# Kernel tuning notes

Hardware: AMD Instinct MI355X
Metric: run time of the kernel (lower is better)

The kernel has to match this reference:

```python
import jax, jax.numpy as jnp
import numpy as np

N_NODES = 50000
N_EDGES = 600000
DIM = 128
VOCAB = 512
PAD_ID = 0
LN_EPS = 1e-5


def setup_inputs() -> dict:
    key = jax.random.key(0)
    ks = jax.random.split(key, 8)
    node_ids = jax.random.randint(ks[0], (N_NODES,), 0, VOCAB, dtype=jnp.int32)
    edge_index = jax.random.randint(ks[1], (2, N_EDGES), 0, N_NODES, dtype=jnp.int32)
    edge_weight = jax.random.uniform(ks[2], (N_EDGES,), dtype=jnp.float32)
    # embedding with padding row zeroed (padding_idx semantics)
    emb = jax.random.normal(ks[3], (VOCAB, DIM), dtype=jnp.float32) * 0.05
    emb = emb.at[PAD_ID].set(0.0)
    s = 1.0 / np.sqrt(DIM)
    W1 = jax.random.normal(ks[4], (DIM, DIM), dtype=jnp.float32) * s
    b1 = jnp.zeros((DIM,), jnp.float32)
    W2 = jax.random.normal(ks[5], (DIM, DIM), dtype=jnp.float32) * s
    b2 = jnp.zeros((DIM,), jnp.float32)
    return {
        "node_ids": node_ids, "edge_index": edge_index, "edge_weight": edge_weight,
        "emb": emb, "W1": W1, "b1": b1, "W2": W2, "b2": b2,
        "gamma1": jnp.ones((DIM,), jnp.float32), "beta1": jnp.zeros((DIM,), jnp.float32),
        "gamma2": jnp.ones((DIM,), jnp.float32), "beta2": jnp.zeros((DIM,), jnp.float32),
    }


def _gcn_conv(x, row, col, ew, W, b, n_nodes):
    """PyG GCNConv: normalize=True, add_self_loops=True, improved=False.
    Aggregation j->i: edge (row=src j, col=dst i)."""
    h = x @ W  # [N, out]
    # add self loops with weight 1
    loop = jnp.arange(n_nodes, dtype=row.dtype)
    row_f = jnp.concatenate([row, loop])
    col_f = jnp.concatenate([col, loop])
    ew_f = jnp.concatenate([ew, jnp.ones((n_nodes,), ew.dtype)])
    # symmetric degree normalization (deg over destination index)
    deg = jax.ops.segment_sum(ew_f, col_f, num_segments=n_nodes)
    dis = jnp.where(deg > 0, jax.lax.rsqrt(jnp.maximum(deg, 1e-12)), 0.0)
    norm = dis[row_f] * ew_f * dis[col_f]  # [E+N]
    msg = norm[:, None] * h[row_f]  # gather + scale  [E+N, out]
    out = jax.ops.segment_sum(msg, col_f, num_segments=n_nodes)  # scatter-add
    return out + b


def _layer_norm(x, gamma, beta):
    mu = jnp.mean(x, axis=-1, keepdims=True)
    var = jnp.mean(jnp.square(x - mu), axis=-1, keepdims=True)
    return (x - mu) * jax.lax.rsqrt(var + LN_EPS) * gamma + beta


def reference(node_ids, edge_index, edge_weight, emb, W1, b1, W2, b2,
              gamma1, beta1, gamma2, beta2):
    row, col = edge_index[0], edge_index[1]
    x = emb[node_ids]  # [N, D]
    x1 = _gcn_conv(x, row, col, edge_weight, W1, b1, N_NODES)
    x = _layer_norm(x + x1, gamma1, beta1)  # dropout is identity in eval
    x2 = _gcn_conv(x, row, col, edge_weight, W2, b2, N_NODES)
    x = _layer_norm(x + x2, gamma2, beta2)
    return x
```

## Files before the change

kernel.cpp:

```cpp
#include <hip/hip_runtime.h>

#define N_NODES 50000
#define N_EDGES 600000
#define DIM     128
#define VOCAB   512
#define LN_EPS  1e-5f
#define FIXS    16777216.0f
#define BCAP    64

typedef unsigned int uint;
typedef unsigned long long ull;
typedef unsigned short ushort;
typedef unsigned char uchar;
typedef __attribute__((ext_vector_type(8))) short s8v;
typedef __attribute__((ext_vector_type(4))) float f4v;
typedef __attribute__((ext_vector_type(4))) int   i4v;
typedef __attribute__((ext_vector_type(4))) uint  u4v;
typedef __attribute__((ext_vector_type(2))) int   i2v;
typedef __attribute__((ext_vector_type(4))) float fv4;
typedef __attribute__((ext_vector_type(2))) float f2v;

__device__ __forceinline__ uint f2bf(float f) {
    uint u = __float_as_uint(f);
    return (u + 0x7fffu + ((u >> 16) & 1u)) >> 16;
}
__device__ __forceinline__ float bf_lo(uint p) { return __uint_as_float(p << 16); }
__device__ __forceinline__ float bf_hi(uint p) { return __uint_as_float(p & 0xffff0000u); }
__device__ __forceinline__ float dis_of(ull pv) {
    return rsqrtf(1.0f + (float)(uint)(pv & 0xffffffffu) * (1.0f / FIXS));
}

__global__ __launch_bounds__(256) void deg_mm1_kernel(
        const int* __restrict__ ei, const float* __restrict__ ew,
        ull* pack, ushort* __restrict__ rank, int E,
        const float* __restrict__ X, const float* __restrict__ W,
        uint* __restrict__ Hb, int M,
        const float* __restrict__ W2, ushort* __restrict__ Wp) {
    __shared__ float Wt[32 * 128];
    __shared__ float Xt[64 * 36];
    int tid = threadIdx.x;
    int nbDeg = (E / 8 + 255) / 256;
    int nmm = (M + 63) / 64;
    if ((int)blockIdx.x < nbDeg) {
        int e0 = (blockIdx.x * 256 + tid) * 8;
        if (e0 >= E) return;
        i4v c0 = __builtin_nontemporal_load((const i4v*)(ei + E + e0));
        i4v c1 = __builtin_nontemporal_load((const i4v*)(ei + E + e0 + 4));
        fv4 w0 = __builtin_nontemporal_load((const fv4*)(ew + e0));
        fv4 w1 = __builtin_nontemporal_load((const fv4*)(ew + e0 + 4));
        int   c[8] = {c0.x, c0.y, c0.z, c0.w, c1.x, c1.y, c1.z, c1.w};
        float w[8] = {w0.x, w0.y, w0.z, w0.w, w1.x, w1.y, w1.z, w1.w};
        ull r[8];
        #pragma unroll
        for (int k = 0; k < 8; k++) {
            ull a = (1ull << 32) | (ull)(uint)__float2int_rn(w[k] * FIXS);
            r[k] = atomicAdd(&pack[c[k]], a);
        }
        u4v o;
        o.x = (uint)(r[0] >> 32) | ((uint)(r[1] >> 32) << 16);
        o.y = (uint)(r[2] >> 32) | ((uint)(r[3] >> 32) << 16);
        o.z = (uint)(r[4] >> 32) | ((uint)(r[5] >> 32) << 16);
        o.w = (uint)(r[6] >> 32) | ((uint)(r[7] >> 32) << 16);
        __builtin_nontemporal_store(o, (u4v*)(rank + e0));
        return;
    }
    if ((int)blockIdx.x >= nbDeg + nmm) {
        int o = (blockIdx.x - nbDeg - nmm) * 256 + tid;
        int j = o & 7, lane = (o >> 3) & 63, chunk = o >> 9;
        int kc = chunk & 3, nc = chunk >> 2;
        int k = kc * 32 + (lane >> 4) * 8 + j;
        int n = nc * 16 + (lane & 15);
        Wp[o] = (ushort)f2bf(W2[k * 128 + n]);
        return;
    }
    int bx = blockIdx.x - nbDeg;
    int tx = tid & 31, ty = tid >> 5;
    int r0 = bx * 64;
    float acc[8][4];
    #pragma unroll
    for (int j = 0; j < 8; j++)
        #pragma unroll
        for (int c = 0; c < 4; c++) acc[j][c] = 0.f;

    for (int kb = 0; kb < 128; kb += 32) {
        __syncthreads();
        #pragma unroll
        for (int q = 0; q < 4; q++) {
            int f = q * 256 + tid;
            ((float4*)Wt)[f] = *(const float4*)(W + kb * 128 + f * 4);
        }
        #pragma unroll
        for (int q = 0; q < 2; q++) {
            int f = q * 256 + tid;
            int row = f >> 3, cs = f & 7;
            int gr = r0 + row;
            float4 xv = make_float4(0.f, 0.f, 0.f, 0.f);
            if (gr < M) xv = *(const float4*)(X + (size_t)gr * 128 + kb + cs * 4);
            *(float4*)(Xt + row * 36 + cs * 4) = xv;
        }
        __syncthreads();
        #pragma unroll
        for (int k = 0; k < 32; k += 4) {
            float wv[4][4];
            #pragma unroll
            for (int kk = 0; kk < 4; kk++) {
                float4 t4 = *(const float4*)(Wt + (k + kk) * 128 + tx * 4);
                wv[kk][0] = t4.x; wv[kk][1] = t4.y; wv[kk][2] = t4.z; wv[kk][3] = t4.w;
            }
            #pragma unroll
            for (int j = 0; j < 8; j++) {
                float4 xv = *(const float4*)(Xt + (ty * 8 + j) * 36 + k);
                float xs[4] = {xv.x, xv.y, xv.z, xv.w};
                #pragma unroll
                for (int kk = 0; kk < 4; kk++)
                    #pragma unroll
                    for (int c = 0; c < 4; c++)
                        acc[j][c] = fmaf(xs[kk], wv[kk][c], acc[j][c]);
            }
        }
    }
    #pragma unroll
    for (int j = 0; j < 8; j++) {
        int gr = r0 + ty * 8 + j;
        if (gr < M) {
            uint p0 = f2bf(acc[j][0]) | (f2bf(acc[j][1]) << 16);
            uint p1 = f2bf(acc[j][2]) | (f2bf(acc[j][3]) << 16);
            ((uint2*)Hb)[(size_t)gr * 32 + tx] = make_uint2(p0, p1);
        }
    }
}

__global__ void scatter_kernel(const int* __restrict__ ei, const float* __restrict__ ew,
                               const ull* __restrict__ pack, const int* __restrict__ nid,
                               const ushort* __restrict__ rank,
                               int2* __restrict__ epack, int E) {
    int e0 = (blockIdx.x * blockDim.x + threadIdx.x) * 4;
    if (e0 >= E) return;
    int4    s4 = *(const int4*)   (ei + e0);
    int4    c4 = *(const int4*)   (ei + E + e0);
    float4  w4 = *(const float4*) (ew + e0);
    ushort4 r4 = *(const ushort4*)(rank + e0);
    int   s[4] = {s4.x, s4.y, s4.z, s4.w};
    int   c[4] = {c4.x, c4.y, c4.z, c4.w};
    float w[4] = {w4.x, w4.y, w4.z, w4.w};
    int   r[4] = {r4.x, r4.y, r4.z, r4.w};
    #pragma unroll
    for (int k = 0; k < 4; k++) {
        ull ps = pack[s[k]];
        float dls = dis_of(ps);
        int pos = c[k] * BCAP + r[k];
        uint ids = (uint)s[k] | ((uint)nid[s[k]] << 16);
        epack[pos] = make_int2((int)ids, __float_as_int(dls * w[k]));
    }
}

__global__ __launch_bounds__(256) void mm2_mfma(const uint* __restrict__ Xb,
                                                const ushort* __restrict__ Wp,
                                                char* __restrict__ H8,
                                                float* __restrict__ rowscale, int M) {
    int wid = (blockIdx.x * 256 + threadIdx.x) >> 6;
    int lane = threadIdx.x & 63;
    int r0 = wid * 16;
    if (r0 >= M) return;
    int quad = lane >> 4, lo = lane & 15;
    const uint* xrow = Xb + (size_t)(r0 + lo) * 64 + quad * 4;
    s8v a[4];
    #pragma unroll
    for (int kc = 0; kc < 4; kc++) a[kc] = *(const s8v*)(xrow + kc * 16);
    f4v acc[8];
    #pragma unroll
    for (int nc = 0; nc < 8; nc++) {
        acc[nc] = (f4v){0.f, 0.f, 0.f, 0.f};
        #pragma unroll
        for (int kc = 0; kc < 4; kc++) {
            s8v b = *(const s8v*)(Wp + (size_t)((nc * 4 + kc) * 64 + lane) * 8);
            acc[nc] = __builtin_amdgcn_mfma_f32_16x16x32_bf16(a[kc], b, acc[nc], 0, 0, 0);
        }
    }
    float m[4];
    #pragma unroll
    for (int r = 0; r < 4; r++) {
        m[r] = 0.f;
        #pragma unroll
        for (int nc = 0; nc < 8; nc++) m[r] = fmaxf(m[r], fabsf(acc[nc][r]));
    }
    #pragma unroll
    for (int o = 1; o <= 8; o <<= 1)
        #pragma unroll
        for (int r = 0; r < 4; r++) m[r] = fmaxf(m[r], __shfl_xor(m[r], o, 64));
    #pragma unroll
    for (int r = 0; r < 4; r++) {
        float inv = (m[r] > 0.f) ? 127.0f / m[r] : 0.f;
        if (lo == 0) rowscale[r0 + quad * 4 + r] = m[r] * (1.0f / 127.0f);
        char* hp = H8 + (size_t)(r0 + quad * 4 + r) * 128 + lo;
        #pragma unroll
        for (int nc = 0; nc < 8; nc++)
            hp[nc * 16] = (char)__float2int_rn(acc[nc][r] * inv);
    }
}

template<int SHIFT, bool RESID_BF, bool OUT_BF, bool GI8>
__global__ __launch_bounds__(256) void agg_ln(const ull* __restrict__ pack,
                                              const int2* __restrict__ epack,
                                              const void* __restrict__ hb,
                                              const float* __restrict__ rowscale,
                                              const int* __restrict__ nid,
                                              const void* __restrict__ resid,
                                              const float* __restrict__ bias,
                                              const float* __restrict__ gamma,
                                              const float* __restrict__ beta,
                                              void* __restrict__ out, int n) {
    int i = (blockIdx.x * 256 + threadIdx.x) >> 6;
    int lane = threadIdx.x & 63;
    if (i >= n) return;
    int iw = __builtin_amdgcn_readfirstlane(i);
    ull pv = pack[iw];
    int deg = (int)(pv >> 32);
    float dl = dis_of(pv);
    int hri = nid ? nid[iw] : iw;
    float slo, shi;
    if (GI8) {
        uint ps = ((const ushort*)hb)[(size_t)hri * 64 + lane];
        float sc = rowscale[hri];
        slo = sc * (float)(signed char)(ps & 0xffu);
        shi = sc * (float)(signed char)(ps >> 8);
    } else {
        uint ps = ((const uint*)hb)[(size_t)hri * 64 + lane];
        slo = bf_lo(ps); shi = bf_hi(ps);
    }
    float sx[4] = {dl * slo, 0.f, 0.f, 0.f};
    float sy[4] = {dl * shi, 0.f, 0.f, 0.f};
    const int2* ep = epack + (size_t)iw * BCAP;
    for (int j = 0; j < deg; j += 8) {
        int2 er[8];
        #pragma unroll
        for (int k = 0; k < 8; k++) {
            int idx = (j + k < deg) ? j + k : deg - 1;
            er[k] = ep[idx];
        }
        uint qv[8];
        float sc[8];
        #pragma unroll
        for (int k = 0; k < 8; k++) {
            size_t row = ((uint)er[k].x >> SHIFT) & 0xffffu;
            if (GI8) {
                qv[k] = ((const ushort*)hb)[row * 64 + lane];
                sc[k] = rowscale[row];
            } else {
                qv[k] = ((const uint*)hb)[row * 64 + lane];
            }
        }
        #pragma unroll
        for (int k = 0; k < 8; k++) {
            float w = (j + k < deg) ? __int_as_float(er[k].y) : 0.f;
            float lo, hi;
            if (GI8) {
                w *= sc[k];
                lo = (float)(signed char)(qv[k] & 0xffu);
                hi = (float)(signed char)(qv[k] >> 8);
            } else {
                lo = bf_lo(qv[k]); hi = bf_hi(qv[k]);
            }
            sx[k & 3] += w * lo;
            sy[k & 3] += w * hi;
        }
    }
    float acc0 = (sx[0] + sx[1]) + (sx[2] + sx[3]);
    float acc1 = (sy[0] + sy[1]) + (sy[2] + sy[3]);
    float2 xr;
    if (RESID_BF) {
        uint pr = __builtin_nontemporal_load((const uint*)resid + (size_t)hri * 64 + lane);
        xr = make_float2(bf_lo(pr), bf_hi(pr));
    } else {
        xr = ((const float2*)resid)[(size_t)hri * 64 + lane];
    }
    float2 bi = ((const float2*)bias)[lane];
    float v0 = xr.x + dl * acc0 + bi.x;
    float v1 = xr.y + dl * acc1 + bi.y;
    float s1 = v0 + v1, s2 = v0 * v0 + v1 * v1;
    #pragma unroll
    for (int o = 32; o > 0; o >>= 1) {
        s1 += __shfl_xor(s1, o, 64);
        s2 += __shfl_xor(s2, o, 64);
    }
    float mu   = s1 * (1.0f / DIM);
    float var  = s2 * (1.0f / DIM) - mu * mu;
    float rstd = rsqrtf(var + LN_EPS);
    float2 ga = ((const float2*)gamma)[lane];
    float2 be = ((const float2*)beta)[lane];
    float o0 = (v0 - mu) * rstd * ga.x + be.x;
    float o1 = (v1 - mu) * rstd * ga.y + be.y;
    if (OUT_BF) {
        __builtin_nontemporal_store(f2bf(o0) | (f2bf(o1) << 16),
                                    (uint*)out + (size_t)i * 64 + lane);
    } else {
        f2v ov = {o0, o1};
        __builtin_nontemporal_store(ov, (f2v*)((float2*)out + (size_t)i * 64 + lane));
    }
}

extern "C" void kernel_launch(void* const* d_in, const int* in_sizes, int n_in,
                              void* d_out, int out_size, void* d_ws, size_t ws_size,
                              hipStream_t stream) {
    const int*   node_ids = (const int*)  d_in[0];
    const int*   ei       = (const int*)  d_in[1];
    const float* ew       = (const float*)d_in[2];
    const float* emb      = (const float*)d_in[3];
    const float* W1       = (const float*)d_in[4];
    const float* b1       = (const float*)d_in[5];
    const float* W2       = (const float*)d_in[6];
    const float* b2       = (const float*)d_in[7];
    const float* g1       = (const float*)d_in[8];
    const float* be1      = (const float*)d_in[9];
    const float* g2       = (const float*)d_in[10];
    const float* be2      = (const float*)d_in[11];
    float* out = (float*)d_out;

    char* p = (char*)d_ws;
    auto alloc = [&](size_t bytes) {
        char* r = p;
        p += (bytes + 255) & ~(size_t)255;
        return r;
    };
    char*   h8      = (char*)  alloc((size_t)N_NODES * DIM);
    float*  rsc     = (float*) alloc((size_t)N_NODES * 4);
    uint*   x1b     = (uint*)  alloc((size_t)N_NODES * 64 * 4);
    uint*   hembB   = (uint*)  alloc((size_t)VOCAB * 64 * 4);
    ushort* Wp      = (ushort*)alloc((size_t)128 * 128 * 2);
    ull*    pack    = (ull*)   alloc((size_t)N_NODES * 8);
    ushort* rank    = (ushort*)alloc((size_t)N_EDGES * 2);
    int2*   epack   = (int2*)  alloc((size_t)N_NODES * BCAP * 8);

    int nbDeg = (N_EDGES / 8 + 255) / 256;
    int nmm = (VOCAB + 63) / 64;

    (void)hipMemsetAsync(pack, 0, (size_t)N_NODES * 8, stream);
    deg_mm1_kernel<<<nbDeg + nmm + 64, 256, 0, stream>>>(
        ei, ew, pack, rank, N_EDGES, emb, W1, hembB, VOCAB, W2, Wp);

    scatter_kernel<<<(N_EDGES / 4 + 255) / 256, 256, 0, stream>>>(
        ei, ew, pack, node_ids, rank, epack, N_EDGES);

    agg_ln<16, false, true, false><<<(N_NODES + 3) / 4, 256, 0, stream>>>(
        pack, epack, hembB, nullptr, node_ids, emb, b1, g1, be1, x1b, N_NODES);

    mm2_mfma<<<(N_NODES / 16 + 3) / 4, 256, 0, stream>>>(x1b, Wp, h8, rsc, N_NODES);
    agg_ln<0, true, false, true><<<(N_NODES + 3) / 4, 256, 0, stream>>>(
        pack, epack, h8, rsc, nullptr, x1b, b2, g2, be2, out, N_NODES);
}
```

Baseline: 213.0 us.

## Fuse edge bucketing into degree atomics and defer source normalization to aggregation

```diff
diff --git a/kernel.cpp b/kernel.cpp
--- a/kernel.cpp
+++ b/kernel.cpp
@@ -15,8 +15,6 @@
 typedef __attribute__((ext_vector_type(8))) short s8v;
 typedef __attribute__((ext_vector_type(4))) float f4v;
 typedef __attribute__((ext_vector_type(4))) int   i4v;
-typedef __attribute__((ext_vector_type(4))) uint  u4v;
-typedef __attribute__((ext_vector_type(2))) int   i2v;
 typedef __attribute__((ext_vector_type(4))) float fv4;
 typedef __attribute__((ext_vector_type(2))) float f2v;
 
@@ -32,36 +30,39 @@
 
 __global__ __launch_bounds__(256) void deg_mm1_kernel(
         const int* __restrict__ ei, const float* __restrict__ ew,
-        ull* pack, ushort* __restrict__ rank, int E,
+        ull* pack, const int* __restrict__ nid, int2* __restrict__ epack, int E,
         const float* __restrict__ X, const float* __restrict__ W,
         uint* __restrict__ Hb, int M,
         const float* __restrict__ W2, ushort* __restrict__ Wp) {
     __shared__ float Wt[32 * 128];
     __shared__ float Xt[64 * 36];
     int tid = threadIdx.x;
-    int nbDeg = (E / 8 + 255) / 256;
+    int nbDeg = (E / 4 + 255) / 256;
     int nmm = (M + 63) / 64;
     if ((int)blockIdx.x < nbDeg) {
-        int e0 = (blockIdx.x * 256 + tid) * 8;
+        int e0 = (blockIdx.x * 256 + tid) * 4;
         if (e0 >= E) return;
-        i4v c0 = __builtin_nontemporal_load((const i4v*)(ei + E + e0));
-        i4v c1 = __builtin_nontemporal_load((const i4v*)(ei + E + e0 + 4));
-        fv4 w0 = __builtin_nontemporal_load((const fv4*)(ew + e0));
-        fv4 w1 = __builtin_nontemporal_load((const fv4*)(ew + e0 + 4));
-        int   c[8] = {c0.x, c0.y, c0.z, c0.w, c1.x, c1.y, c1.z, c1.w};
-        float w[8] = {w0.x, w0.y, w0.z, w0.w, w1.x, w1.y, w1.z, w1.w};
-        ull r[8];
-        #pragma unroll
-        for (int k = 0; k < 8; k++) {
+        i4v s4 = __builtin_nontemporal_load((const i4v*)(ei + e0));
+        i4v c4 = __builtin_nontemporal_load((const i4v*)(ei + E + e0));
+        fv4 w4 = __builtin_nontemporal_load((const fv4*)(ew + e0));
+        int   s[4] = {s4.x, s4.y, s4.z, s4.w};
+        int   c[4] = {c4.x, c4.y, c4.z, c4.w};
+        float w[4] = {w4.x, w4.y, w4.z, w4.w};
+        int nv[4];
+        #pragma unroll
+        for (int k = 0; k < 4; k++) nv[k] = nid[s[k]];
+        ull r[4];
+        #pragma unroll
+        for (int k = 0; k < 4; k++) {
             ull a = (1ull << 32) | (ull)(uint)__float2int_rn(w[k] * FIXS);
             r[k] = atomicAdd(&pack[c[k]], a);
         }
-        u4v o;
-        o.x = (uint)(r[0] >> 32) | ((uint)(r[1] >> 32) << 16);
-        o.y = (uint)(r[2] >> 32) | ((uint)(r[3] >> 32) << 16);
-        o.z = (uint)(r[4] >> 32) | ((uint)(r[5] >> 32) << 16);
-        o.w = (uint)(r[6] >> 32) | ((uint)(r[7] >> 32) << 16);
-        __builtin_nontemporal_store(o, (u4v*)(rank + e0));
+        #pragma unroll
+        for (int k = 0; k < 4; k++) {
+            int rk = (int)(uint)(r[k] >> 32);
+            epack[(size_t)c[k] * BCAP + rk] =
+                make_int2(s[k] | (nv[k] << 16), __float_as_int(w[k]));
+        }
         return;
     }
     if ((int)blockIdx.x >= nbDeg + nmm) {
@@ -130,32 +131,9 @@
     }
 }
 
-__global__ void scatter_kernel(const int* __restrict__ ei, const float* __restrict__ ew,
-                               const ull* __restrict__ pack, const int* __restrict__ nid,
-                               const ushort* __restrict__ rank,
-                               int2* __restrict__ epack, int E) {
-    int e0 = (blockIdx.x * blockDim.x + threadIdx.x) * 4;
-    if (e0 >= E) return;
-    int4    s4 = *(const int4*)   (ei + e0);
-    int4    c4 = *(const int4*)   (ei + E + e0);
-    float4  w4 = *(const float4*) (ew + e0);
-    ushort4 r4 = *(const ushort4*)(rank + e0);
-    int   s[4] = {s4.x, s4.y, s4.z, s4.w};
-    int   c[4] = {c4.x, c4.y, c4.z, c4.w};
-    float w[4] = {w4.x, w4.y, w4.z, w4.w};
-    int   r[4] = {r4.x, r4.y, r4.z, r4.w};
-    #pragma unroll
-    for (int k = 0; k < 4; k++) {
-        ull ps = pack[s[k]];
-        float dls = dis_of(ps);
-        int pos = c[k] * BCAP + r[k];
-        uint ids = (uint)s[k] | ((uint)nid[s[k]] << 16);
-        epack[pos] = make_int2((int)ids, __float_as_int(dls * w[k]));
-    }
-}
-
 __global__ __launch_bounds__(256) void mm2_mfma(const uint* __restrict__ Xb,
                                                 const ushort* __restrict__ Wp,
+                                                const ull* __restrict__ pack,
                                                 char* __restrict__ H8,
                                                 float* __restrict__ rowscale, int M) {
     int wid = (blockIdx.x * 256 + threadIdx.x) >> 6;
@@ -191,7 +169,10 @@
     #pragma unroll
     for (int r = 0; r < 4; r++) {
         float inv = (m[r] > 0.f) ? 127.0f / m[r] : 0.f;
-        if (lo == 0) rowscale[r0 + quad * 4 + r] = m[r] * (1.0f / 127.0f);
+        if (lo == 0) {
+            int rr = r0 + quad * 4 + r;
+            rowscale[rr] = m[r] * (1.0f / 127.0f) * dis_of(pack[rr]);
+        }
         char* hp = H8 + (size_t)(r0 + quad * 4 + r) * 128 + lo;
         #pragma unroll
         for (int nc = 0; nc < 8; nc++)
@@ -199,7 +180,7 @@
     }
 }
 
-template<int SHIFT, bool RESID_BF, bool OUT_BF, bool GI8>
+template<int SHIFT, bool RESID_BF, bool OUT_BF, bool GI8, bool EDGE_DIS>
 __global__ __launch_bounds__(256) void agg_ln(const ull* __restrict__ pack,
                                               const int2* __restrict__ epack,
                                               const void* __restrict__ hb,
@@ -228,8 +209,8 @@
         uint ps = ((const uint*)hb)[(size_t)hri * 64 + lane];
         slo = bf_lo(ps); shi = bf_hi(ps);
     }
-    float sx[4] = {dl * slo, 0.f, 0.f, 0.f};
-    float sy[4] = {dl * shi, 0.f, 0.f, 0.f};
+    float sx[4] = {GI8 ? slo : dl * slo, 0.f, 0.f, 0.f};
+    float sy[4] = {GI8 ? shi : dl * shi, 0.f, 0.f, 0.f};
     const int2* ep = epack + (size_t)iw * BCAP;
     for (int j = 0; j < deg; j += 8) {
         int2 er[8];
@@ -242,12 +223,15 @@
         float sc[8];
         #pragma unroll
         for (int k = 0; k < 8; k++) {
-            size_t row = ((uint)er[k].x >> SHIFT) & 0xffffu;
+            uint ex = (uint)er[k].x;
+            size_t row = (ex >> SHIFT) & 0xffffu;
             if (GI8) {
                 qv[k] = ((const ushort*)hb)[row * 64 + lane];
                 sc[k] = rowscale[row];
             } else {
                 qv[k] = ((const uint*)hb)[row * 64 + lane];
+                if (EDGE_DIS)
+                    sc[k] = (float)((const uint*)pack)[2 * (size_t)(ex & 0xffffu)];
             }
         }
         #pragma unroll
@@ -259,6 +243,7 @@
                 lo = (float)(signed char)(qv[k] & 0xffu);
                 hi = (float)(signed char)(qv[k] >> 8);
             } else {
+                if (EDGE_DIS) w *= rsqrtf(1.0f + sc[k] * (1.0f / FIXS));
                 lo = bf_lo(qv[k]); hi = bf_hi(qv[k]);
             }
             sx[k & 3] += w * lo;
@@ -328,23 +313,19 @@
     uint*   hembB   = (uint*)  alloc((size_t)VOCAB * 64 * 4);
     ushort* Wp      = (ushort*)alloc((size_t)128 * 128 * 2);
     ull*    pack    = (ull*)   alloc((size_t)N_NODES * 8);
-    ushort* rank    = (ushort*)alloc((size_t)N_EDGES * 2);
     int2*   epack   = (int2*)  alloc((size_t)N_NODES * BCAP * 8);
 
-    int nbDeg = (N_EDGES / 8 + 255) / 256;
+    int nbDeg = (N_EDGES / 4 + 255) / 256;
     int nmm = (VOCAB + 63) / 64;
 
     (void)hipMemsetAsync(pack, 0, (size_t)N_NODES * 8, stream);
     deg_mm1_kernel<<<nbDeg + nmm + 64, 256, 0, stream>>>(
-        ei, ew, pack, rank, N_EDGES, emb, W1, hembB, VOCAB, W2, Wp);
-
-    scatter_kernel<<<(N_EDGES / 4 + 255) / 256, 256, 0, stream>>>(
-        ei, ew, pack, node_ids, rank, epack, N_EDGES);
-
-    agg_ln<16, false, true, false><<<(N_NODES + 3) / 4, 256, 0, stream>>>(
+        ei, ew, pack, node_ids, epack, N_EDGES, emb, W1, hembB, VOCAB, W2, Wp);
+
+    agg_ln<16, false, true, false, true><<<(N_NODES + 3) / 4, 256, 0, stream>>>(
         pack, epack, hembB, nullptr, node_ids, emb, b1, g1, be1, x1b, N_NODES);
 
-    mm2_mfma<<<(N_NODES / 16 + 3) / 4, 256, 0, stream>>>(x1b, Wp, h8, rsc, N_NODES);
-    agg_ln<0, true, false, true><<<(N_NODES + 3) / 4, 256, 0, stream>>>(
+    mm2_mfma<<<(N_NODES / 16 + 3) / 4, 256, 0, stream>>>(x1b, Wp, pack, h8, rsc, N_NODES);
+    agg_ln<0, true, false, true, false><<<(N_NODES + 3) / 4, 256, 0, stream>>>(
         pack, epack, h8, rsc, nullptr, x1b, b2, g2, be2, out, N_NODES);
 }
```

After: 212.4 us. Within noise of the previous version (-0.3%).
